# Kernel tuning notes

Measured on AMD Instinct MI355X. Metric: run time of the kernel, lower is better.

Reference implementation:

```python
import jax, jax.numpy as jnp
import numpy as np

H = 8            # num heads
K_ORDER = 3      # polynomial filter order


def setup_inputs() -> dict:
    key = jax.random.key(0)
    ks = jax.random.split(key, 7)
    B, N, D = 4, 2048, 256
    s = 0.05  # weight scale to keep softmax/poly numerically tame
    x = jax.random.normal(ks[0], (B, N, D), jnp.float32)
    Wq = jax.random.normal(ks[1], (D, D), jnp.float32) * s
    Wk = jax.random.normal(ks[2], (D, D), jnp.float32) * s
    Wv = jax.random.normal(ks[3], (D, D), jnp.float32) * s
    Wo = jax.random.normal(ks[4], (D, D), jnp.float32) * s
    coeffs = jax.random.normal(ks[5], (H, K_ORDER + 1), jnp.float32) * 0.5
    z = jnp.zeros((D,), jnp.float32)
    return {"x": x, "Wq": Wq, "bq": z, "Wk": Wk, "bk": z,
            "Wv": Wv, "bv": z, "Wo": Wo, "bo": z, "coeffs": coeffs}


def reference(x, Wq, bq, Wk, bk, Wv, bv, Wo, bo, coeffs):
    B, N, D = x.shape
    hd = D // H

    def split_heads(t):  # [B,N,D] -> [B,H,N,hd]
        return t.reshape(B, N, H, hd).transpose(0, 2, 1, 3)

    q = split_heads(x @ Wq + bq)
    k = split_heads(x @ Wk + bk)
    v = split_heads(x @ Wv + bv)

    # Estimator: learned adjacency via scaled-dot-product softmax, [B,H,N,N]
    scale = jnp.asarray(1.0 / np.sqrt(hd), x.dtype)
    A = jax.nn.softmax(jnp.einsum('bhnd,bhmd->bhnm', q, k) * scale, axis=-1)

    # Filter: X' = sum_{k=0}^{K} c[h,k] * A^k V
    out = coeffs[None, :, 0, None, None] * v
    t = v
    for kk in range(1, K_ORDER + 1):
        t = jnp.einsum('bhnm,bhmd->bhnd', A, t)
        out = out + coeffs[None, :, kk, None, None] * t

    merged = out.transpose(0, 2, 1, 3).reshape(B, N, D)  # concat heads
    return merged @ Wo + bo
```

## Files before the change

### kernel.cpp

```cpp
#include <hip/hip_runtime.h>
#include <hip/hip_bf16.h>

typedef __hip_bfloat16 bf16;
typedef __attribute__((ext_vector_type(8))) short short8;
typedef __attribute__((ext_vector_type(4))) short short4v;
typedef __attribute__((ext_vector_type(4))) float f32x4;

#define BB 4
#define NN 2048
#define DD 256
#define HH 8
#define HD 32
#define BN (BB*NN)
#define ELEMS (BN*DD)

__device__ int g_isf32;
__device__ __attribute__((aligned(256))) unsigned short g_qb [ELEMS];
__device__ __attribute__((aligned(256))) unsigned short g_kb [ELEMS];
__device__ __attribute__((aligned(256))) unsigned short g_tA [ELEMS];
__device__ __attribute__((aligned(256))) unsigned short g_tB [ELEMS];
__device__ __attribute__((aligned(256))) float          g_acc[ELEMS];
__device__ __attribute__((aligned(256))) unsigned short g_wt [4*DD*DD];
__device__ __attribute__((aligned(256))) float g_bias[4*DD];
__device__ __attribute__((aligned(256))) float g_cf[HH*4];

__device__ __forceinline__ float b2f(unsigned short u) {
    union { unsigned int i; float f; } c; c.i = ((unsigned int)u) << 16; return c.f;
}
__device__ __forceinline__ unsigned short f2b(float f) {
    bf16 h = __float2bfloat16(f);
    return *reinterpret_cast<unsigned short*>(&h);
}
#if __has_builtin(__builtin_amdgcn_cvt_pk_bf16_f32)
typedef __attribute__((ext_vector_type(2))) __bf16 bf16x2t;
__device__ __forceinline__ unsigned int pk2(float a, float b) {
    union { bf16x2t v; unsigned int u; } c;
    c.v = __builtin_amdgcn_cvt_pk_bf16_f32(a, b);
    return c.u;
}
#else
__device__ __forceinline__ unsigned int pk2(float a, float b) {
    unsigned int ua = __float_as_uint(a), ub = __float_as_uint(b);
    ua = (ua + 0x7FFFu + ((ua >> 16) & 1u)) >> 16;
    ub = (ub + 0x7FFFu + ((ub >> 16) & 1u)) & 0xFFFF0000u;
    return ua | ub;
}
#endif
__device__ __forceinline__ float ldin(const void* p, int i, int f32m) {
    return f32m ? ((const float*)p)[i] : b2f(((const unsigned short*)p)[i]);
}

__global__ __launch_bounds__(256) void probe_kernel(const void* __restrict__ x)
{
    __shared__ int cnt;
    if (threadIdx.x == 0) cnt = 0;
    __syncthreads();
    const unsigned short* u = (const unsigned short*)x;
    int w = 0;
    for (int i = threadIdx.x; i < 1024; i += 256) {
        const int e = (u[2 * i] >> 7) & 0xFF;
        if (e < 100 || e > 140) ++w;
    }
    atomicAdd(&cnt, w);
    __syncthreads();
    if (threadIdx.x == 0) g_isf32 = (cnt > 300) ? 1 : 0;
}

__global__ __launch_bounds__(256) void prep_w_kernel(
    const void* W0, const void* W1, const void* W2, const void* W3,
    const void* bq, const void* bk, const void* bv, const void* bo,
    const void* coeffs)
{
    const int f32m = g_isf32;
    __shared__ unsigned short tile[64][65];
    const int mat = blockIdx.y;
    const void* W = (mat == 0) ? W0 : (mat == 1) ? W1 : (mat == 2) ? W2 : W3;
    const int k0 = (blockIdx.x >> 2) * 64;
    const int n0 = (blockIdx.x & 3) * 64;
    const int t  = threadIdx.x;

    if (blockIdx.x == 0 && blockIdx.y == 0) {
        g_bias[0 * DD + t] = ldin(bq, t, f32m);
        g_bias[1 * DD + t] = ldin(bk, t, f32m);
        g_bias[2 * DD + t] = ldin(bv, t, f32m);
        g_bias[3 * DD + t] = ldin(bo, t, f32m);
        if (t < 32) g_cf[t] = ldin(coeffs, t, f32m);
    }

    #pragma unroll
    for (int it = 0; it < 16; ++it) {
        const int flat = it * 256 + t;
        const int i = flat >> 6, j = flat & 63;
        tile[j][i] = f2b(ldin(W, (k0 + i) * DD + n0 + j, f32m));
    }
    __syncthreads();
    unsigned short* wt = g_wt + mat * DD * DD;
    #pragma unroll
    for (int it = 0; it < 16; ++it) {
        const int flat = it * 256 + t;
        const int nl = flat >> 6, kl = flat & 63;
        wt[(n0 + nl) * DD + k0 + kl] = tile[nl][kl];
    }
}

__global__ __launch_bounds__(256) void qkv_gemm_kernel(const void* __restrict__ x)
{
    __shared__ unsigned short xs[64 * 32];
    __shared__ unsigned short wl[64 * 32];
    const int f32m = g_isf32;
    const int t  = threadIdx.x;
    const int w  = t >> 6, l = t & 63, lg = l >> 4, ln = l & 15;
    const int r0 = blockIdx.x * 64;
    const int n0 = blockIdx.y * 64;
    const int mat = blockIdx.z;
    const unsigned short* wt = g_wt + mat * DD * DD;
    const int sr = t >> 2, sc = (t & 3) * 8;

    f32x4 acc[4] = {{0,0,0,0},{0,0,0,0},{0,0,0,0},{0,0,0,0}};

    for (int kc = 0; kc < DD; kc += 32) {
        __syncthreads();
        if (f32m) {
            const float* src = (const float*)x + (size_t)(r0 + sr) * DD + kc + sc;
            const float4 a = *(const float4*)src;
            const float4 b = *(const float4*)(src + 4);
            union { uint4 v; unsigned short s[8]; } o;
            o.s[0]=f2b(a.x); o.s[1]=f2b(a.y); o.s[2]=f2b(a.z); o.s[3]=f2b(a.w);
            o.s[4]=f2b(b.x); o.s[5]=f2b(b.y); o.s[6]=f2b(b.z); o.s[7]=f2b(b.w);
            *(uint4*)(xs + sr * 32 + sc) = o.v;
        } else {
            *(uint4*)(xs + sr * 32 + sc) =
                *(const uint4*)((const unsigned short*)x + (size_t)(r0 + sr) * DD + kc + sc);
        }
        *(uint4*)(wl + sr * 32 + sc) =
            *(const uint4*)(wt + (size_t)(n0 + sr) * DD + kc + sc);
        __syncthreads();
        const short8 af = *(const short8*)(xs + (w * 16 + ln) * 32 + lg * 8);
        #pragma unroll
        for (int s = 0; s < 4; ++s) {
            const short8 bfr = *(const short8*)(wl + (s * 16 + ln) * 32 + lg * 8);
            acc[s] = __builtin_amdgcn_mfma_f32_16x16x32_bf16(af, bfr, acc[s], 0, 0, 0);
        }
    }

    const float QS = 0.17677669529663687f * 1.4426950408889634f;
    #pragma unroll
    for (int s = 0; s < 4; ++s) {
        const int j = n0 + s * 16 + ln;
        const float bias = g_bias[mat * DD + j];
        const int h = j >> 5, dd = j & 31;
        #pragma unroll
        for (int r = 0; r < 4; ++r) {
            const int rn = r0 + w * 16 + lg * 4 + r;
            const int b = rn >> 11, n = rn & (NN - 1);
            const int bh = b * HH + h;
            const float val = acc[s][r] + bias;
            if (mat == 0) {
                g_qb[((size_t)bh * NN + n) * HD + dd] = f2b(val * QS);
            } else if (mat == 1) {
                g_kb[((size_t)bh * NN + n) * HD + dd] = f2b(val);
            } else {
                g_tA[((size_t)bh * HD + dd) * NN + n] = f2b(val);
                g_acc[(size_t)rn * DD + j] = g_cf[h * 4] * val;
            }
        }
    }
}

__global__ __launch_bounds__(256) void attn_pass_kernel(const int kidx, const int dir)
{
    __shared__ float osh[4][64][33];
    __shared__ float lsh[4][64];

    const unsigned short* __restrict__ tin  = dir ? g_tB : g_tA;
    unsigned short*       __restrict__ tout = dir ? g_tA : g_tB;

    const int tid = threadIdx.x;
    const int w   = tid >> 6;
    const int l   = tid & 63;
    const int lg  = l >> 4;
    const int ln  = l & 15;

    const int bh = blockIdx.x >> 5;
    const int qt = blockIdx.x & 31;
    const int h  = bh & (HH - 1);
    const int b  = bh >> 3;
    const int q0 = qt * 64;

    short8 qf[4];
    #pragma unroll
    for (int qi = 0; qi < 4; ++qi)
        qf[qi] = *(const short8*)(g_qb +
            ((size_t)bh * NN + q0 + qi * 16 + ln) * HD + lg * 8);

    const unsigned short* kb = g_kb + (size_t)bh * NN * HD;
    const unsigned short* tb = tin  + (size_t)bh * HD * NN;

    f32x4 oacc[4][2];
    #pragma unroll
    for (int qi = 0; qi < 4; ++qi) { oacc[qi][0] = (f32x4){0,0,0,0}; oacc[qi][1] = (f32x4){0,0,0,0}; }
    float lsum[4] = {0.f, 0.f, 0.f, 0.f};
    const f32x4 zero = {0.f, 0.f, 0.f, 0.f};

    for (int it = 0; it < 16; ++it) {
        const int k0 = it * 128 + w * 32;
        const short8 kf0 = *(const short8*)(kb + (size_t)(k0 + ln) * HD + lg * 8);
        const short8 kf1 = *(const short8*)(kb + (size_t)(k0 + 16 + ln) * HD + lg * 8);

#if __has_builtin(__builtin_amdgcn_mfma_f32_16x16x16bf16_1k)
        short4v tf[2][2];
        #pragma unroll
        for (int c = 0; c < 2; ++c)
            #pragma unroll
            for (int hf = 0; hf < 2; ++hf)
                tf[c][hf] = *(const short4v*)(tb +
                    (size_t)(hf * 16 + ln) * NN + k0 + c * 16 + lg * 4);

        #pragma unroll
        for (int qi = 0; qi < 4; ++qi) {
            f32x4 s0 = __builtin_amdgcn_mfma_f32_16x16x32_bf16(kf0, qf[qi], zero, 0, 0, 0);
            f32x4 s1 = __builtin_amdgcn_mfma_f32_16x16x32_bf16(kf1, qf[qi], zero, 0, 0, 0);
            float p[8];
            #pragma unroll
            for (int r = 0; r < 4; ++r) {
                p[r]     = __builtin_amdgcn_exp2f(s0[r]);
                p[4 + r] = __builtin_amdgcn_exp2f(s1[r]);
                lsum[qi] += p[r] + p[4 + r];
            }
            union { unsigned int u[2]; short4v s; } pb0, pb1;
            pb0.u[0] = pk2(p[0], p[1]); pb0.u[1] = pk2(p[2], p[3]);
            pb1.u[0] = pk2(p[4], p[5]); pb1.u[1] = pk2(p[6], p[7]);
            oacc[qi][0] = __builtin_amdgcn_mfma_f32_16x16x16bf16_1k(tf[0][0], pb0.s, oacc[qi][0], 0, 0, 0);
            oacc[qi][1] = __builtin_amdgcn_mfma_f32_16x16x16bf16_1k(tf[0][1], pb0.s, oacc[qi][1], 0, 0, 0);
            oacc[qi][0] = __builtin_amdgcn_mfma_f32_16x16x16bf16_1k(tf[1][0], pb1.s, oacc[qi][0], 0, 0, 0);
            oacc[qi][1] = __builtin_amdgcn_mfma_f32_16x16x16bf16_1k(tf[1][1], pb1.s, oacc[qi][1], 0, 0, 0);
        }
#else
        const short8 tf0 = *(const short8*)(tb + (size_t)ln * NN + k0 + lg * 8);
        const short8 tf1 = *(const short8*)(tb + (size_t)(ln + 16) * NN + k0 + lg * 8);
        #pragma unroll
        for (int qi = 0; qi < 4; ++qi) {
            f32x4 s0 = __builtin_amdgcn_mfma_f32_16x16x32_bf16(kf0, qf[qi], zero, 0, 0, 0);
            f32x4 s1 = __builtin_amdgcn_mfma_f32_16x16x32_bf16(kf1, qf[qi], zero, 0, 0, 0);
            float p[8];
            #pragma unroll
            for (int r = 0; r < 4; ++r) {
                p[r]     = __builtin_amdgcn_exp2f(s0[r]);
                p[4 + r] = __builtin_amdgcn_exp2f(s1[r]);
                lsum[qi] += p[r] + p[4 + r];
            }
            const unsigned int pk0 = pk2(p[0], p[1]);
            const unsigned int pk1 = pk2(p[2], p[3]);
            const unsigned int pk2v = pk2(p[4], p[5]);
            const unsigned int pk3 = pk2(p[6], p[7]);
            int bi[4];
            #pragma unroll
            for (int j = 0; j < 4; ++j) {
                const int srcLane = (((2 * lg + (j >> 1)) & 3) << 4) + ln;
                const int lo = __shfl((j & 1) ? (int)pk1 : (int)pk0, srcLane, 64);
                const int hi = __shfl((j & 1) ? (int)pk3 : (int)pk2v, srcLane, 64);
                bi[j] = (lg < 2) ? lo : hi;
            }
            union { int i[4]; short8 s; } pf;
            pf.i[0] = bi[0]; pf.i[1] = bi[1]; pf.i[2] = bi[2]; pf.i[3] = bi[3];
            oacc[qi][0] = __builtin_amdgcn_mfma_f32_16x16x32_bf16(tf0, pf.s, oacc[qi][0], 0, 0, 0);
            oacc[qi][1] = __builtin_amdgcn_mfma_f32_16x16x32_bf16(tf1, pf.s, oacc[qi][1], 0, 0, 0);
        }
#endif
    }

    #pragma unroll
    for (int qi = 0; qi < 4; ++qi) {
        lsum[qi] += __shfl_xor(lsum[qi], 16, 64);
        lsum[qi] += __shfl_xor(lsum[qi], 32, 64);
    }
    if (lg == 0) {
        #pragma unroll
        for (int qi = 0; qi < 4; ++qi) lsh[w][qi * 16 + ln] = lsum[qi];
    }

    #pragma unroll
    for (int qi = 0; qi < 4; ++qi)
        #pragma unroll
        for (int hf = 0; hf < 2; ++hf)
            #pragma unroll
            for (int r = 0; r < 4; ++r)
                osh[w][qi * 16 + ln][hf * 16 + lg * 4 + r] = oacc[qi][hf][r];
    __syncthreads();

    {
        const int q  = tid & 63;
        const int db = (tid >> 6) * 8;
        const float invl = 1.0f / (lsh[0][q] + lsh[1][q] + lsh[2][q] + lsh[3][q]);
        const float ck = g_cf[h * 4 + kidx];
        #pragma unroll
        for (int dd = 0; dd < 8; ++dd) {
            const int d = db + dd;
            const float val = (osh[0][q][d] + osh[1][q][d] +
                               osh[2][q][d] + osh[3][q][d]) * invl;
            tout[((size_t)bh * HD + d) * NN + q0 + q] = f2b(val);
            float* ga = g_acc + ((size_t)(b * NN + q0 + q)) * DD + h * HD + d;
            *ga += ck * val;
        }
    }
}

__global__ __launch_bounds__(256) void out_gemm_kernel(void* __restrict__ out)
{
    __shared__ unsigned short xs[64 * 32];
    __shared__ unsigned short wl[64 * 32];
    const int f32m = g_isf32;
    const int t  = threadIdx.x;
    const int w  = t >> 6, l = t & 63, lg = l >> 4, ln = l & 15;
    const int r0 = blockIdx.x * 64;
    const int n0 = blockIdx.y * 64;
    const unsigned short* wt = g_wt + 3 * DD * DD;
    const int sr = t >> 2, sc = (t & 3) * 8;

    f32x4 acc[4] = {{0,0,0,0},{0,0,0,0},{0,0,0,0},{0,0,0,0}};

    for (int kc = 0; kc < DD; kc += 32) {
        __syncthreads();
        {
            const float* src = g_acc + (size_t)(r0 + sr) * DD + kc + sc;
            const float4 a = *(const float4*)src;
            const float4 b = *(const float4*)(src + 4);
            union { uint4 v; unsigned short s[8]; } o;
            o.s[0]=f2b(a.x); o.s[1]=f2b(a.y); o.s[2]=f2b(a.z); o.s[3]=f2b(a.w);
            o.s[4]=f2b(b.x); o.s[5]=f2b(b.y); o.s[6]=f2b(b.z); o.s[7]=f2b(b.w);
            *(uint4*)(xs + sr * 32 + sc) = o.v;
        }
        *(uint4*)(wl + sr * 32 + sc) =
            *(const uint4*)(wt + (size_t)(n0 + sr) * DD + kc + sc);
        __syncthreads();
        const short8 af = *(const short8*)(xs + (w * 16 + ln) * 32 + lg * 8);
        #pragma unroll
        for (int s = 0; s < 4; ++s) {
            const short8 bfr = *(const short8*)(wl + (s * 16 + ln) * 32 + lg * 8);
            acc[s] = __builtin_amdgcn_mfma_f32_16x16x32_bf16(af, bfr, acc[s], 0, 0, 0);
        }
    }

    #pragma unroll
    for (int s = 0; s < 4; ++s) {
        const int j = n0 + s * 16 + ln;
        const float bias = g_bias[3 * DD + j];
        #pragma unroll
        for (int r = 0; r < 4; ++r) {
            const int rn = r0 + w * 16 + lg * 4 + r;
            const float val = acc[s][r] + bias;
            if (f32m) ((float*)out)[(size_t)rn * DD + j] = val;
            else      ((bf16*)out)[(size_t)rn * DD + j] = __float2bfloat16(val);
        }
    }
}

extern "C" void kernel_launch(void* const* d_in, const int* in_sizes, int n_in,
                              void* d_out, int out_size, void* d_ws, size_t ws_size,
                              hipStream_t stream)
{
    const void* x      = d_in[0];
    const void* Wq     = d_in[1];
    const void* bq     = d_in[2];
    const void* Wk     = d_in[3];
    const void* bk     = d_in[4];
    const void* Wv     = d_in[5];
    const void* bv     = d_in[6];
    const void* Wo     = d_in[7];
    const void* bo     = d_in[8];
    const void* coeffs = d_in[9];
    (void)d_ws; (void)ws_size; (void)in_sizes; (void)n_in; (void)out_size;

    probe_kernel<<<1, 256, 0, stream>>>(x);

    prep_w_kernel<<<dim3(16, 4), 256, 0, stream>>>(Wq, Wk, Wv, Wo,
                                                   bq, bk, bv, bo, coeffs);

    qkv_gemm_kernel<<<dim3(128, 4, 3), 256, 0, stream>>>(x);

    const int agrid = (BB * HH) * (NN / 64);
    attn_pass_kernel<<<agrid, 256, 0, stream>>>(1, 0);
    attn_pass_kernel<<<agrid, 256, 0, stream>>>(2, 1);
    attn_pass_kernel<<<agrid, 256, 0, stream>>>(3, 0);

    out_gemm_kernel<<<dim3(128, 4), 256, 0, stream>>>(d_out);
}
```

Before: 241.6 us.

## Reuse softmax row sums across passes, prefetch K/T tiles, skip final T store

Result: slower. 248.6 us (+2.9%).

```diff
diff --git a/kernel.cpp b/kernel.cpp
--- a/kernel.cpp
+++ b/kernel.cpp
@@ -23,6 +23,7 @@
 __device__ __attribute__((aligned(256))) unsigned short g_wt [4*DD*DD];
 __device__ __attribute__((aligned(256))) float g_bias[4*DD];
 __device__ __attribute__((aligned(256))) float g_cf[HH*4];
+__device__ __attribute__((aligned(256))) float g_invl[BB*HH*NN];
 
 __device__ __forceinline__ float b2f(unsigned short u) {
     union { unsigned int i; float f; } c; c.i = ((unsigned int)u) << 16; return c.f;
@@ -167,6 +168,7 @@
     }
 }
 
+template<int KIND>
 __global__ __launch_bounds__(256) void attn_pass_kernel(const int kidx, const int dir)
 {
     __shared__ float osh[4][64][33];
@@ -196,25 +198,36 @@
     const unsigned short* kb = g_kb + (size_t)bh * NN * HD;
     const unsigned short* tb = tin  + (size_t)bh * HD * NN;
 
+    const f32x4 zero = {0.f, 0.f, 0.f, 0.f};
     f32x4 oacc[4][2];
     #pragma unroll
-    for (int qi = 0; qi < 4; ++qi) { oacc[qi][0] = (f32x4){0,0,0,0}; oacc[qi][1] = (f32x4){0,0,0,0}; }
-    float lsum[4] = {0.f, 0.f, 0.f, 0.f};
-    const f32x4 zero = {0.f, 0.f, 0.f, 0.f};
-
+    for (int qi = 0; qi < 4; ++qi) { oacc[qi][0] = zero; oacc[qi][1] = zero; }
+    f32x4 sacc[4];
+    if (KIND == 0) {
+        #pragma unroll
+        for (int qi = 0; qi < 4; ++qi) sacc[qi] = zero;
+    }
+
+#if __has_builtin(__builtin_amdgcn_mfma_f32_16x16x16bf16_1k)
+    const short4v vone = {16256, 16256, 16256, 16256};
+
+    const int kw = w * 32;
+    short8  kf0  = *(const short8*) (kb + (size_t)(kw + ln) * HD + lg * 8);
+    short8  kf1  = *(const short8*) (kb + (size_t)(kw + 16 + ln) * HD + lg * 8);
+    short4v tf00 = *(const short4v*)(tb + (size_t)(ln)      * NN + kw +      lg * 4);
+    short4v tf01 = *(const short4v*)(tb + (size_t)(16 + ln) * NN + kw +      lg * 4);
+    short4v tf10 = *(const short4v*)(tb + (size_t)(ln)      * NN + kw + 16 + lg * 4);
+    short4v tf11 = *(const short4v*)(tb + (size_t)(16 + ln) * NN + kw + 16 + lg * 4);
+
+    #pragma unroll 2
     for (int it = 0; it < 16; ++it) {
-        const int k0 = it * 128 + w * 32;
-        const short8 kf0 = *(const short8*)(kb + (size_t)(k0 + ln) * HD + lg * 8);
-        const short8 kf1 = *(const short8*)(kb + (size_t)(k0 + 16 + ln) * HD + lg * 8);
-
-#if __has_builtin(__builtin_amdgcn_mfma_f32_16x16x16bf16_1k)
-        short4v tf[2][2];
-        #pragma unroll
-        for (int c = 0; c < 2; ++c)
-            #pragma unroll
-            for (int hf = 0; hf < 2; ++hf)
-                tf[c][hf] = *(const short4v*)(tb +
-                    (size_t)(hf * 16 + ln) * NN + k0 + c * 16 + lg * 4);
+        const int k0n = ((it < 15) ? (it + 1) * 128 : 0) + kw;
+        short8  nkf0  = *(const short8*) (kb + (size_t)(k0n + ln) * HD + lg * 8);
+        short8  nkf1  = *(const short8*) (kb + (size_t)(k0n + 16 + ln) * HD + lg * 8);
+        short4v ntf00 = *(const short4v*)(tb + (size_t)(ln)      * NN + k0n +      lg * 4);
+        short4v ntf01 = *(const short4v*)(tb + (size_t)(16 + ln) * NN + k0n +      lg * 4);
+        short4v ntf10 = *(const short4v*)(tb + (size_t)(ln)      * NN + k0n + 16 + lg * 4);
+        short4v ntf11 = *(const short4v*)(tb + (size_t)(16 + ln) * NN + k0n + 16 + lg * 4);
 
         #pragma unroll
         for (int qi = 0; qi < 4; ++qi) {
@@ -225,17 +238,33 @@
             for (int r = 0; r < 4; ++r) {
                 p[r]     = __builtin_amdgcn_exp2f(s0[r]);
                 p[4 + r] = __builtin_amdgcn_exp2f(s1[r]);
-                lsum[qi] += p[r] + p[4 + r];
             }
             union { unsigned int u[2]; short4v s; } pb0, pb1;
             pb0.u[0] = pk2(p[0], p[1]); pb0.u[1] = pk2(p[2], p[3]);
             pb1.u[0] = pk2(p[4], p[5]); pb1.u[1] = pk2(p[6], p[7]);
-            oacc[qi][0] = __builtin_amdgcn_mfma_f32_16x16x16bf16_1k(tf[0][0], pb0.s, oacc[qi][0], 0, 0, 0);
-            oacc[qi][1] = __builtin_amdgcn_mfma_f32_16x16x16bf16_1k(tf[0][1], pb0.s, oacc[qi][1], 0, 0, 0);
-            oacc[qi][0] = __builtin_amdgcn_mfma_f32_16x16x16bf16_1k(tf[1][0], pb1.s, oacc[qi][0], 0, 0, 0);
-            oacc[qi][1] = __builtin_amdgcn_mfma_f32_16x16x16bf16_1k(tf[1][1], pb1.s, oacc[qi][1], 0, 0, 0);
-        }
+            if (KIND == 0) {
+                sacc[qi] = __builtin_amdgcn_mfma_f32_16x16x16bf16_1k(vone, pb0.s, sacc[qi], 0, 0, 0);
+                sacc[qi] = __builtin_amdgcn_mfma_f32_16x16x16bf16_1k(vone, pb1.s, sacc[qi], 0, 0, 0);
+            }
+            oacc[qi][0] = __builtin_amdgcn_mfma_f32_16x16x16bf16_1k(tf00, pb0.s, oacc[qi][0], 0, 0, 0);
+            oacc[qi][1] = __builtin_amdgcn_mfma_f32_16x16x16bf16_1k(tf01, pb0.s, oacc[qi][1], 0, 0, 0);
+            oacc[qi][0] = __builtin_amdgcn_mfma_f32_16x16x16bf16_1k(tf10, pb1.s, oacc[qi][0], 0, 0, 0);
+            oacc[qi][1] = __builtin_amdgcn_mfma_f32_16x16x16bf16_1k(tf11, pb1.s, oacc[qi][1], 0, 0, 0);
+        }
+        kf0 = nkf0; kf1 = nkf1;
+        tf00 = ntf00; tf01 = ntf01; tf10 = ntf10; tf11 = ntf11;
+    }
+
+    if (KIND == 0 && lg == 0) {
+        #pragma unroll
+        for (int qi = 0; qi < 4; ++qi) lsh[w][qi * 16 + ln] = sacc[qi][0];
+    }
 #else
+    float lsum[4] = {0.f, 0.f, 0.f, 0.f};
+    for (int it = 0; it < 16; ++it) {
+        const int k0 = it * 128 + w * 32;
+        const short8 kf0 = *(const short8*)(kb + (size_t)(k0 + ln) * HD + lg * 8);
+        const short8 kf1 = *(const short8*)(kb + (size_t)(k0 + 16 + ln) * HD + lg * 8);
         const short8 tf0 = *(const short8*)(tb + (size_t)ln * NN + k0 + lg * 8);
         const short8 tf1 = *(const short8*)(tb + (size_t)(ln + 16) * NN + k0 + lg * 8);
         #pragma unroll
@@ -266,18 +295,19 @@
             oacc[qi][0] = __builtin_amdgcn_mfma_f32_16x16x32_bf16(tf0, pf.s, oacc[qi][0], 0, 0, 0);
             oacc[qi][1] = __builtin_amdgcn_mfma_f32_16x16x32_bf16(tf1, pf.s, oacc[qi][1], 0, 0, 0);
         }
+    }
+    if (KIND == 0) {
+        #pragma unroll
+        for (int qi = 0; qi < 4; ++qi) {
+            lsum[qi] += __shfl_xor(lsum[qi], 16, 64);
+            lsum[qi] += __shfl_xor(lsum[qi], 32, 64);
+        }
+        if (lg == 0) {
+            #pragma unroll
+            for (int qi = 0; qi < 4; ++qi) lsh[w][qi * 16 + ln] = lsum[qi];
+        }
+    }
 #endif
-    }
-
-    #pragma unroll
-    for (int qi = 0; qi < 4; ++qi) {
-        lsum[qi] += __shfl_xor(lsum[qi], 16, 64);
-        lsum[qi] += __shfl_xor(lsum[qi], 32, 64);
-    }
-    if (lg == 0) {
-        #pragma unroll
-        for (int qi = 0; qi < 4; ++qi) lsh[w][qi * 16 + ln] = lsum[qi];
-    }
 
     #pragma unroll
     for (int qi = 0; qi < 4; ++qi)
@@ -291,14 +321,21 @@
     {
         const int q  = tid & 63;
         const int db = (tid >> 6) * 8;
-        const float invl = 1.0f / (lsh[0][q] + lsh[1][q] + lsh[2][q] + lsh[3][q]);
+        float invl;
+        if (KIND == 0) {
+            invl = 1.0f / (lsh[0][q] + lsh[1][q] + lsh[2][q] + lsh[3][q]);
+            if (db == 0) g_invl[(size_t)bh * NN + q0 + q] = invl;
+        } else {
+            invl = g_invl[(size_t)bh * NN + q0 + q];
+        }
         const float ck = g_cf[h * 4 + kidx];
         #pragma unroll
         for (int dd = 0; dd < 8; ++dd) {
             const int d = db + dd;
             const float val = (osh[0][q][d] + osh[1][q][d] +
                                osh[2][q][d] + osh[3][q][d]) * invl;
-            tout[((size_t)bh * HD + d) * NN + q0 + q] = f2b(val);
+            if (KIND != 2)
+                tout[((size_t)bh * HD + d) * NN + q0 + q] = f2b(val);
             float* ga = g_acc + ((size_t)(b * NN + q0 + q)) * DD + h * HD + d;
             *ga += ck * val;
         }
@@ -379,9 +416,9 @@
     qkv_gemm_kernel<<<dim3(128, 4, 3), 256, 0, stream>>>(x);
 
     const int agrid = (BB * HH) * (NN / 64);
-    attn_pass_kernel<<<agrid, 256, 0, stream>>>(1, 0);
-    attn_pass_kernel<<<agrid, 256, 0, stream>>>(2, 1);
-    attn_pass_kernel<<<agrid, 256, 0, stream>>>(3, 0);
+    attn_pass_kernel<0><<<agrid, 256, 0, stream>>>(1, 0);
+    attn_pass_kernel<1><<<agrid, 256, 0, stream>>>(2, 1);
+    attn_pass_kernel<2><<<agrid, 256, 0, stream>>>(3, 0);
 
     out_gemm_kernel<<<dim3(128, 4), 256, 0, stream>>>(d_out);
 }
```

## Halve attention query tile, compute softmax sums once, skip final t write

Applied to the files above, without the earlier changes.

Result: slower. 361.6 us (+49.7%).

```diff
diff --git a/kernel.cpp b/kernel.cpp
--- a/kernel.cpp
+++ b/kernel.cpp
@@ -23,6 +23,7 @@
 __device__ __attribute__((aligned(256))) unsigned short g_wt [4*DD*DD];
 __device__ __attribute__((aligned(256))) float g_bias[4*DD];
 __device__ __attribute__((aligned(256))) float g_cf[HH*4];
+__device__ __attribute__((aligned(256))) float g_invl[BB*HH*NN];
 
 __device__ __forceinline__ float b2f(unsigned short u) {
     union { unsigned int i; float f; } c; c.i = ((unsigned int)u) << 16; return c.f;
@@ -167,10 +168,11 @@
     }
 }
 
-__global__ __launch_bounds__(256) void attn_pass_kernel(const int kidx, const int dir)
-{
-    __shared__ float osh[4][64][33];
-    __shared__ float lsh[4][64];
+template<int KIND>
+__global__ __launch_bounds__(256, 6) void attn_pass_kernel(const int kidx, const int dir)
+{
+    __shared__ float osh[4][32][33];
+    __shared__ float lsh[4][32];
 
     const unsigned short* __restrict__ tin  = dir ? g_tB : g_tA;
     unsigned short*       __restrict__ tout = dir ? g_tA : g_tB;
@@ -181,33 +183,36 @@
     const int lg  = l >> 4;
     const int ln  = l & 15;
 
-    const int bh = blockIdx.x >> 5;
-    const int qt = blockIdx.x & 31;
+    const int bh = blockIdx.x >> 6;
+    const int qt = blockIdx.x & 63;
     const int h  = bh & (HH - 1);
     const int b  = bh >> 3;
-    const int q0 = qt * 64;
-
-    short8 qf[4];
-    #pragma unroll
-    for (int qi = 0; qi < 4; ++qi)
+    const int q0 = qt * 32;
+
+    short8 qf[2];
+    #pragma unroll
+    for (int qi = 0; qi < 2; ++qi)
         qf[qi] = *(const short8*)(g_qb +
             ((size_t)bh * NN + q0 + qi * 16 + ln) * HD + lg * 8);
 
     const unsigned short* kb = g_kb + (size_t)bh * NN * HD;
     const unsigned short* tb = tin  + (size_t)bh * HD * NN;
 
-    f32x4 oacc[4][2];
-    #pragma unroll
-    for (int qi = 0; qi < 4; ++qi) { oacc[qi][0] = (f32x4){0,0,0,0}; oacc[qi][1] = (f32x4){0,0,0,0}; }
-    float lsum[4] = {0.f, 0.f, 0.f, 0.f};
     const f32x4 zero = {0.f, 0.f, 0.f, 0.f};
+    f32x4 oacc[2][2];
+    #pragma unroll
+    for (int qi = 0; qi < 2; ++qi) { oacc[qi][0] = zero; oacc[qi][1] = zero; }
+    f32x4 sacc[2];
+    if (KIND == 0) { sacc[0] = zero; sacc[1] = zero; }
+
+#if __has_builtin(__builtin_amdgcn_mfma_f32_16x16x16bf16_1k)
+    const short4v vone = {16256, 16256, 16256, 16256};
 
     for (int it = 0; it < 16; ++it) {
         const int k0 = it * 128 + w * 32;
         const short8 kf0 = *(const short8*)(kb + (size_t)(k0 + ln) * HD + lg * 8);
         const short8 kf1 = *(const short8*)(kb + (size_t)(k0 + 16 + ln) * HD + lg * 8);
 
-#if __has_builtin(__builtin_amdgcn_mfma_f32_16x16x16bf16_1k)
         short4v tf[2][2];
         #pragma unroll
         for (int c = 0; c < 2; ++c)
@@ -217,7 +222,7 @@
                     (size_t)(hf * 16 + ln) * NN + k0 + c * 16 + lg * 4);
 
         #pragma unroll
-        for (int qi = 0; qi < 4; ++qi) {
+        for (int qi = 0; qi < 2; ++qi) {
             f32x4 s0 = __builtin_amdgcn_mfma_f32_16x16x32_bf16(kf0, qf[qi], zero, 0, 0, 0);
             f32x4 s1 = __builtin_amdgcn_mfma_f32_16x16x32_bf16(kf1, qf[qi], zero, 0, 0, 0);
             float p[8];
@@ -225,21 +230,35 @@
             for (int r = 0; r < 4; ++r) {
                 p[r]     = __builtin_amdgcn_exp2f(s0[r]);
                 p[4 + r] = __builtin_amdgcn_exp2f(s1[r]);
-                lsum[qi] += p[r] + p[4 + r];
             }
             union { unsigned int u[2]; short4v s; } pb0, pb1;
             pb0.u[0] = pk2(p[0], p[1]); pb0.u[1] = pk2(p[2], p[3]);
             pb1.u[0] = pk2(p[4], p[5]); pb1.u[1] = pk2(p[6], p[7]);
+            if (KIND == 0) {
+                sacc[qi] = __builtin_amdgcn_mfma_f32_16x16x16bf16_1k(vone, pb0.s, sacc[qi], 0, 0, 0);
+                sacc[qi] = __builtin_amdgcn_mfma_f32_16x16x16bf16_1k(vone, pb1.s, sacc[qi], 0, 0, 0);
+            }
             oacc[qi][0] = __builtin_amdgcn_mfma_f32_16x16x16bf16_1k(tf[0][0], pb0.s, oacc[qi][0], 0, 0, 0);
             oacc[qi][1] = __builtin_amdgcn_mfma_f32_16x16x16bf16_1k(tf[0][1], pb0.s, oacc[qi][1], 0, 0, 0);
             oacc[qi][0] = __builtin_amdgcn_mfma_f32_16x16x16bf16_1k(tf[1][0], pb1.s, oacc[qi][0], 0, 0, 0);
             oacc[qi][1] = __builtin_amdgcn_mfma_f32_16x16x16bf16_1k(tf[1][1], pb1.s, oacc[qi][1], 0, 0, 0);
         }
+    }
+
+    if (KIND == 0 && lg == 0) {
+        #pragma unroll
+        for (int qi = 0; qi < 2; ++qi) lsh[w][qi * 16 + ln] = sacc[qi][0];
+    }
 #else
+    float lsum[2] = {0.f, 0.f};
+    for (int it = 0; it < 16; ++it) {
+        const int k0 = it * 128 + w * 32;
+        const short8 kf0 = *(const short8*)(kb + (size_t)(k0 + ln) * HD + lg * 8);
+        const short8 kf1 = *(const short8*)(kb + (size_t)(k0 + 16 + ln) * HD + lg * 8);
         const short8 tf0 = *(const short8*)(tb + (size_t)ln * NN + k0 + lg * 8);
         const short8 tf1 = *(const short8*)(tb + (size_t)(ln + 16) * NN + k0 + lg * 8);
         #pragma unroll
-        for (int qi = 0; qi < 4; ++qi) {
+        for (int qi = 0; qi < 2; ++qi) {
             f32x4 s0 = __builtin_amdgcn_mfma_f32_16x16x32_bf16(kf0, qf[qi], zero, 0, 0, 0);
             f32x4 s1 = __builtin_amdgcn_mfma_f32_16x16x32_bf16(kf1, qf[qi], zero, 0, 0, 0);
             float p[8];
@@ -266,21 +285,22 @@
             oacc[qi][0] = __builtin_amdgcn_mfma_f32_16x16x32_bf16(tf0, pf.s, oacc[qi][0], 0, 0, 0);
             oacc[qi][1] = __builtin_amdgcn_mfma_f32_16x16x32_bf16(tf1, pf.s, oacc[qi][1], 0, 0, 0);
         }
+    }
+    if (KIND == 0) {
+        #pragma unroll
+        for (int qi = 0; qi < 2; ++qi) {
+            lsum[qi] += __shfl_xor(lsum[qi], 16, 64);
+            lsum[qi] += __shfl_xor(lsum[qi], 32, 64);
+        }
+        if (lg == 0) {
+            #pragma unroll
+            for (int qi = 0; qi < 2; ++qi) lsh[w][qi * 16 + ln] = lsum[qi];
+        }
+    }
 #endif
-    }
-
-    #pragma unroll
-    for (int qi = 0; qi < 4; ++qi) {
-        lsum[qi] += __shfl_xor(lsum[qi], 16, 64);
-        lsum[qi] += __shfl_xor(lsum[qi], 32, 64);
-    }
-    if (lg == 0) {
-        #pragma unroll
-        for (int qi = 0; qi < 4; ++qi) lsh[w][qi * 16 + ln] = lsum[qi];
-    }
-
-    #pragma unroll
-    for (int qi = 0; qi < 4; ++qi)
+
+    #pragma unroll
+    for (int qi = 0; qi < 2; ++qi)
         #pragma unroll
         for (int hf = 0; hf < 2; ++hf)
             #pragma unroll
@@ -289,16 +309,23 @@
     __syncthreads();
 
     {
-        const int q  = tid & 63;
-        const int db = (tid >> 6) * 8;
-        const float invl = 1.0f / (lsh[0][q] + lsh[1][q] + lsh[2][q] + lsh[3][q]);
+        const int q  = tid & 31;
+        const int db = (tid >> 5) * 4;
+        float invl;
+        if (KIND == 0) {
+            invl = 1.0f / (lsh[0][q] + lsh[1][q] + lsh[2][q] + lsh[3][q]);
+            if (db == 0) g_invl[(size_t)bh * NN + q0 + q] = invl;
+        } else {
+            invl = g_invl[(size_t)bh * NN + q0 + q];
+        }
         const float ck = g_cf[h * 4 + kidx];
         #pragma unroll
-        for (int dd = 0; dd < 8; ++dd) {
+        for (int dd = 0; dd < 4; ++dd) {
             const int d = db + dd;
             const float val = (osh[0][q][d] + osh[1][q][d] +
                                osh[2][q][d] + osh[3][q][d]) * invl;
-            tout[((size_t)bh * HD + d) * NN + q0 + q] = f2b(val);
+            if (KIND != 2)
+                tout[((size_t)bh * HD + d) * NN + q0 + q] = f2b(val);
             float* ga = g_acc + ((size_t)(b * NN + q0 + q)) * DD + h * HD + d;
             *ga += ck * val;
         }
@@ -378,10 +405,10 @@
 
     qkv_gemm_kernel<<<dim3(128, 4, 3), 256, 0, stream>>>(x);
 
-    const int agrid = (BB * HH) * (NN / 64);
-    attn_pass_kernel<<<agrid, 256, 0, stream>>>(1, 0);
-    attn_pass_kernel<<<agrid, 256, 0, stream>>>(2, 1);
-    attn_pass_kernel<<<agrid, 256, 0, stream>>>(3, 0);
+    const int agrid = (BB * HH) * (NN / 32);
+    attn_pass_kernel<0><<<agrid, 256, 0, stream>>>(1, 0);
+    attn_pass_kernel<1><<<agrid, 256, 0, stream>>>(2, 1);
+    attn_pass_kernel<2><<<agrid, 256, 0, stream>>>(3, 0);
 
     out_gemm_kernel<<<dim3(128, 4), 256, 0, stream>>>(d_out);
 }
```

## Cache softmax row sums across passes and widen per-iteration key tile

Applied to the files above, without the earlier changes.

Result: slower. 281.0 us (+16.3%).

```diff
diff --git a/kernel.cpp b/kernel.cpp
--- a/kernel.cpp
+++ b/kernel.cpp
@@ -23,6 +23,7 @@
 __device__ __attribute__((aligned(256))) unsigned short g_wt [4*DD*DD];
 __device__ __attribute__((aligned(256))) float g_bias[4*DD];
 __device__ __attribute__((aligned(256))) float g_cf[HH*4];
+__device__ __attribute__((aligned(256))) float g_invl[BB*HH*NN];
 
 __device__ __forceinline__ float b2f(unsigned short u) {
     union { unsigned int i; float f; } c; c.i = ((unsigned int)u) << 16; return c.f;
@@ -167,7 +168,8 @@
     }
 }
 
-__global__ __launch_bounds__(256) void attn_pass_kernel(const int kidx, const int dir)
+template<int KIND>
+__global__ __launch_bounds__(256, 4) void attn_pass_kernel(const int kidx, const int dir)
 {
     __shared__ float osh[4][64][33];
     __shared__ float lsh[4][64];
@@ -196,46 +198,60 @@
     const unsigned short* kb = g_kb + (size_t)bh * NN * HD;
     const unsigned short* tb = tin  + (size_t)bh * HD * NN;
 
+    const f32x4 zero = {0.f, 0.f, 0.f, 0.f};
     f32x4 oacc[4][2];
     #pragma unroll
-    for (int qi = 0; qi < 4; ++qi) { oacc[qi][0] = (f32x4){0,0,0,0}; oacc[qi][1] = (f32x4){0,0,0,0}; }
+    for (int qi = 0; qi < 4; ++qi) { oacc[qi][0] = zero; oacc[qi][1] = zero; }
     float lsum[4] = {0.f, 0.f, 0.f, 0.f};
-    const f32x4 zero = {0.f, 0.f, 0.f, 0.f};
-
+
+#if __has_builtin(__builtin_amdgcn_mfma_f32_16x16x16bf16_1k)
+    for (int it = 0; it < 8; ++it) {
+        const int k0 = it * 256 + w * 64;
+
+        short8 kf[4];
+        #pragma unroll
+        for (int c = 0; c < 4; ++c)
+            kf[c] = *(const short8*)(kb + (size_t)(k0 + c * 16 + ln) * HD + lg * 8);
+
+        short4v tf[4][2];
+        #pragma unroll
+        for (int c = 0; c < 4; ++c)
+            #pragma unroll
+            for (int hf = 0; hf < 2; ++hf)
+                tf[c][hf] = *(const short4v*)(tb +
+                    (size_t)(hf * 16 + ln) * NN + k0 + c * 16 + lg * 4);
+
+        #pragma unroll
+        for (int qi = 0; qi < 4; ++qi) {
+            f32x4 s[4];
+            #pragma unroll
+            for (int c = 0; c < 4; ++c)
+                s[c] = __builtin_amdgcn_mfma_f32_16x16x32_bf16(kf[c], qf[qi], zero, 0, 0, 0);
+            float p[16];
+            #pragma unroll
+            for (int c = 0; c < 4; ++c)
+                #pragma unroll
+                for (int r = 0; r < 4; ++r)
+                    p[c * 4 + r] = __builtin_amdgcn_exp2f(s[c][r]);
+            if (KIND == 0) {
+                #pragma unroll
+                for (int e = 0; e < 16; ++e) lsum[qi] += p[e];
+            }
+            #pragma unroll
+            for (int c = 0; c < 4; ++c) {
+                union { unsigned int u[2]; short4v s; } pb;
+                pb.u[0] = pk2(p[c * 4 + 0], p[c * 4 + 1]);
+                pb.u[1] = pk2(p[c * 4 + 2], p[c * 4 + 3]);
+                oacc[qi][0] = __builtin_amdgcn_mfma_f32_16x16x16bf16_1k(tf[c][0], pb.s, oacc[qi][0], 0, 0, 0);
+                oacc[qi][1] = __builtin_amdgcn_mfma_f32_16x16x16bf16_1k(tf[c][1], pb.s, oacc[qi][1], 0, 0, 0);
+            }
+        }
+    }
+#else
     for (int it = 0; it < 16; ++it) {
         const int k0 = it * 128 + w * 32;
         const short8 kf0 = *(const short8*)(kb + (size_t)(k0 + ln) * HD + lg * 8);
         const short8 kf1 = *(const short8*)(kb + (size_t)(k0 + 16 + ln) * HD + lg * 8);
-
-#if __has_builtin(__builtin_amdgcn_mfma_f32_16x16x16bf16_1k)
-        short4v tf[2][2];
-        #pragma unroll
-        for (int c = 0; c < 2; ++c)
-            #pragma unroll
-            for (int hf = 0; hf < 2; ++hf)
-                tf[c][hf] = *(const short4v*)(tb +
-                    (size_t)(hf * 16 + ln) * NN + k0 + c * 16 + lg * 4);
-
-        #pragma unroll
-        for (int qi = 0; qi < 4; ++qi) {
-            f32x4 s0 = __builtin_amdgcn_mfma_f32_16x16x32_bf16(kf0, qf[qi], zero, 0, 0, 0);
-            f32x4 s1 = __builtin_amdgcn_mfma_f32_16x16x32_bf16(kf1, qf[qi], zero, 0, 0, 0);
-            float p[8];
-            #pragma unroll
-            for (int r = 0; r < 4; ++r) {
-                p[r]     = __builtin_amdgcn_exp2f(s0[r]);
-                p[4 + r] = __builtin_amdgcn_exp2f(s1[r]);
-                lsum[qi] += p[r] + p[4 + r];
-            }
-            union { unsigned int u[2]; short4v s; } pb0, pb1;
-            pb0.u[0] = pk2(p[0], p[1]); pb0.u[1] = pk2(p[2], p[3]);
-            pb1.u[0] = pk2(p[4], p[5]); pb1.u[1] = pk2(p[6], p[7]);
-            oacc[qi][0] = __builtin_amdgcn_mfma_f32_16x16x16bf16_1k(tf[0][0], pb0.s, oacc[qi][0], 0, 0, 0);
-            oacc[qi][1] = __builtin_amdgcn_mfma_f32_16x16x16bf16_1k(tf[0][1], pb0.s, oacc[qi][1], 0, 0, 0);
-            oacc[qi][0] = __builtin_amdgcn_mfma_f32_16x16x16bf16_1k(tf[1][0], pb1.s, oacc[qi][0], 0, 0, 0);
-            oacc[qi][1] = __builtin_amdgcn_mfma_f32_16x16x16bf16_1k(tf[1][1], pb1.s, oacc[qi][1], 0, 0, 0);
-        }
-#else
         const short8 tf0 = *(const short8*)(tb + (size_t)ln * NN + k0 + lg * 8);
         const short8 tf1 = *(const short8*)(tb + (size_t)(ln + 16) * NN + k0 + lg * 8);
         #pragma unroll
@@ -266,17 +282,19 @@
             oacc[qi][0] = __builtin_amdgcn_mfma_f32_16x16x32_bf16(tf0, pf.s, oacc[qi][0], 0, 0, 0);
             oacc[qi][1] = __builtin_amdgcn_mfma_f32_16x16x32_bf16(tf1, pf.s, oacc[qi][1], 0, 0, 0);
         }
+    }
 #endif
-    }
-
-    #pragma unroll
-    for (int qi = 0; qi < 4; ++qi) {
-        lsum[qi] += __shfl_xor(lsum[qi], 16, 64);
-        lsum[qi] += __shfl_xor(lsum[qi], 32, 64);
-    }
-    if (lg == 0) {
-        #pragma unroll
-        for (int qi = 0; qi < 4; ++qi) lsh[w][qi * 16 + ln] = lsum[qi];
+
+    if (KIND == 0) {
+        #pragma unroll
+        for (int qi = 0; qi < 4; ++qi) {
+            lsum[qi] += __shfl_xor(lsum[qi], 16, 64);
+            lsum[qi] += __shfl_xor(lsum[qi], 32, 64);
+        }
+        if (lg == 0) {
+            #pragma unroll
+            for (int qi = 0; qi < 4; ++qi) lsh[w][qi * 16 + ln] = lsum[qi];
+        }
     }
 
     #pragma unroll
@@ -291,14 +309,21 @@
     {
         const int q  = tid & 63;
         const int db = (tid >> 6) * 8;
-        const float invl = 1.0f / (lsh[0][q] + lsh[1][q] + lsh[2][q] + lsh[3][q]);
+        float invl;
+        if (KIND == 0) {
+            invl = 1.0f / (lsh[0][q] + lsh[1][q] + lsh[2][q] + lsh[3][q]);
+            if (db == 0) g_invl[(size_t)bh * NN + q0 + q] = invl;
+        } else {
+            invl = g_invl[(size_t)bh * NN + q0 + q];
+        }
         const float ck = g_cf[h * 4 + kidx];
         #pragma unroll
         for (int dd = 0; dd < 8; ++dd) {
             const int d = db + dd;
             const float val = (osh[0][q][d] + osh[1][q][d] +
                                osh[2][q][d] + osh[3][q][d]) * invl;
-            tout[((size_t)bh * HD + d) * NN + q0 + q] = f2b(val);
+            if (KIND != 2)
+                tout[((size_t)bh * HD + d) * NN + q0 + q] = f2b(val);
             float* ga = g_acc + ((size_t)(b * NN + q0 + q)) * DD + h * HD + d;
             *ga += ck * val;
         }
@@ -379,9 +404,9 @@
     qkv_gemm_kernel<<<dim3(128, 4, 3), 256, 0, stream>>>(x);
 
     const int agrid = (BB * HH) * (NN / 64);
-    attn_pass_kernel<<<agrid, 256, 0, stream>>>(1, 0);
-    attn_pass_kernel<<<agrid, 256, 0, stream>>>(2, 1);
-    attn_pass_kernel<<<agrid, 256, 0, stream>>>(3, 0);
+    attn_pass_kernel<0><<<agrid, 256, 0, stream>>>(1, 0);
+    attn_pass_kernel<1><<<agrid, 256, 0, stream>>>(2, 1);
+    attn_pass_kernel<2><<<agrid, 256, 0, stream>>>(3, 0);
 
     out_gemm_kernel<<<dim3(128, 4), 256, 0, stream>>>(d_out);
 }
```
